# Kernel optimization log

Measured on AMD Instinct MI355X. Metric: run time of the kernel, lower is better.

Reference implementation:

```python
import jax, jax.numpy as jnp
import numpy as np

N_NODES = 100000
N_EDGES = 1600000
N_GRAPHS = 64
IN_DIM = 128
HIDDEN = 64
OUT_DIM = 6


def gcn_conv(x, W, b, src, dst, n_nodes):
    """PyG GCNConv: D^{-1/2} (A + I) D^{-1/2} X W + b (self-loops added)."""
    xw = x @ W  # [N, H]
    # degree including self-loop (computed over destination nodes)
    deg = jax.ops.segment_sum(jnp.ones((src.shape[0],), xw.dtype), dst,
                              num_segments=n_nodes) + 1.0
    dinv = jax.lax.rsqrt(deg)  # deg >= 1, always safe
    # per-edge normalized messages, scatter-add into destinations
    coef = (dinv[src] * dinv[dst])[:, None]  # [E, 1]
    agg = jax.ops.segment_sum(xw[src] * coef, dst, num_segments=n_nodes)
    # self-loop contribution: dinv[i]^2 * xw[i]
    agg = agg + xw * (dinv * dinv)[:, None]
    return agg + b


def setup_inputs() -> dict:
    key = jax.random.key(0)
    ks = jax.random.split(key, 9)
    x = jax.random.normal(ks[0], (N_NODES, IN_DIM), dtype=jnp.float32)
    edge_index = jax.random.randint(ks[1], (2, N_EDGES), 0, N_NODES, dtype=jnp.int64)
    batch = jnp.sort(jax.random.randint(ks[2], (N_NODES,), 0, N_GRAPHS, dtype=jnp.int64))
    # Glorot-ish params
    W1 = jax.random.normal(ks[3], (IN_DIM, HIDDEN), dtype=jnp.float32) / np.sqrt(IN_DIM)
    b1 = jnp.zeros((HIDDEN,), jnp.float32)
    W2 = jax.random.normal(ks[4], (HIDDEN, HIDDEN), dtype=jnp.float32) / np.sqrt(HIDDEN)
    b2 = jnp.zeros((HIDDEN,), jnp.float32)
    Wl = jax.random.normal(ks[5], (HIDDEN, OUT_DIM), dtype=jnp.float32) / np.sqrt(HIDDEN)
    bl = jnp.zeros((OUT_DIM,), jnp.float32)
    return {"x": x, "edge_index": edge_index, "batch": batch,
            "W1": W1, "b1": b1, "W2": W2, "b2": b2, "Wl": Wl, "bl": bl}


def reference(x, edge_index, batch, W1, b1, W2, b2, Wl, bl):
    src, dst = edge_index[0], edge_index[1]
    h = jax.nn.relu(gcn_conv(x, W1, b1, src, dst, N_NODES))
    # dropout is identity in eval mode
    h = gcn_conv(h, W2, b2, src, dst, N_NODES)
    # global mean pool over graph ids
    sums = jax.ops.segment_sum(h, batch, num_segments=N_GRAPHS)  # [G, H]
    cnts = jax.ops.segment_sum(jnp.ones((h.shape[0],), h.dtype), batch,
                               num_segments=N_GRAPHS)
    pooled = sums / jnp.maximum(cnts, 1.0)[:, None]
    return pooled @ Wl + bl  # [G, OUT_DIM]
```

## Files before the change

### kernel.cpp

```cpp
#include <hip/hip_runtime.h>

#define NCOL 64
#define BSH 8
#define NBMAX 512
#define EPB 2048
#define P2CAP 6144


__device__ __forceinline__ unsigned int bf16pair(float a, float b) {
  unsigned int ua = __float_as_uint(a), ub = __float_as_uint(b);
  ua = (ua + 0x7FFFu + ((ua >> 16) & 1u)) >> 16;
  ub = (ub + 0x7FFFu + ((ub >> 16) & 1u)) >> 16;
  return (ub << 16) | ua;
}
__device__ __forceinline__ float bf_lo(unsigned int v) { return __uint_as_float(v << 16); }
__device__ __forceinline__ float bf_hi(unsigned int v) { return __uint_as_float(v & 0xFFFF0000u); }


__global__ __launch_bounds__(256) void bin_p1(const int* __restrict__ src,
                                              const int* __restrict__ dst,
                                              unsigned int* __restrict__ ent,
                                              int* __restrict__ blockOff,
                                              int ne, int nb) {
  __shared__ int hist[NBMAX];
  __shared__ int base[NBMAX];
  __shared__ int part[256];
  __shared__ unsigned int stage[EPB];
  int tid = threadIdx.x;
  int e0 = blockIdx.x * EPB;
  int cnt = min(EPB, ne - e0);

  for (int i = tid; i < NBMAX; i += 256) hist[i] = 0;
  __syncthreads();
  for (int i = tid; i < cnt; i += 256) {
    int d = dst[e0 + i];
    atomicAdd(&hist[d >> BSH], 1);
  }
  __syncthreads();

  int a0 = hist[2 * tid], a1 = hist[2 * tid + 1];
  int s = a0 + a1;
  part[tid] = s;
  __syncthreads();
  for (int d = 1; d < 256; d <<= 1) {
    int v = (tid >= d) ? part[tid - d] : 0;
    __syncthreads();
    part[tid] += v;
    __syncthreads();
  }
  int off = part[tid] - s;
  base[2 * tid] = off;
  base[2 * tid + 1] = off + a0;
  __syncthreads();

  for (int b = tid; b < nb; b += 256) blockOff[(size_t)blockIdx.x * nb + b] = base[b];
  for (int i = tid; i < NBMAX; i += 256) hist[i] = base[i];
  __syncthreads();

  for (int i = tid; i < cnt; i += 256) {
    int d = dst[e0 + i];
    int sv = src[e0 + i];
    unsigned int e = ((unsigned int)(d & ((1 << BSH) - 1)) << 17) | (unsigned int)sv;
    int p = atomicAdd(&hist[d >> BSH], 1);
    stage[p] = e;
  }
  __syncthreads();
  for (int i = tid; i < cnt; i += 256) ent[e0 + i] = stage[i];
}


__global__ __launch_bounds__(256) void deg_bin(const unsigned int* __restrict__ ent,
                                               const int* __restrict__ blockOff,
                                               int* __restrict__ degi,
                                               int n, int ne, int nb, int nblk) {
  __shared__ int cnt[256];
  int b = blockIdx.x;
  int tid = threadIdx.x;
  cnt[tid] = 0;
  __syncthreads();
  for (int blk = tid; blk < nblk; blk += 256) {
    int e0 = blk * EPB;
    int bcnt = min(EPB, ne - e0);
    int st = blockOff[(size_t)blk * nb + b];
    int en = (b + 1 < nb) ? blockOff[(size_t)blk * nb + b + 1] : bcnt;
    for (int i = st; i < en; ++i) {
      unsigned int e = ent[e0 + i];
      atomicAdd(&cnt[e >> 17], 1);
    }
  }
  __syncthreads();
  int node = (b << BSH) + tid;
  if (node < n) degi[node] = cnt[tid];
}

__global__ void dinv_kernel(const int* __restrict__ degi, float* __restrict__ dinv, int n) {
  int i = blockIdx.x * blockDim.x + threadIdx.x;
  if (i < n) dinv[i] = rsqrtf((float)degi[i] + 1.0f);
}


__global__ void bounds_kernel(const int* __restrict__ batch, int* __restrict__ startg,
                              int* __restrict__ endg, int n) {
  int i = blockIdx.x * blockDim.x + threadIdx.x;
  if (i >= n) return;
  int b = batch[i];
  if (i == 0) {
    startg[b] = 0;
  } else {
    int bp = batch[i - 1];
    if (b != bp) { startg[b] = i; endg[bp] = i; }
  }
  if (i == n - 1) endg[b] = n;
}


#define SCAN_C 8

__global__ void scan_part(const int* __restrict__ degi, int* __restrict__ tsum,
                          int n, int nthreads) {
  int t = blockIdx.x * blockDim.x + threadIdx.x;
  if (t >= nthreads) return;
  int lo = t * SCAN_C, hi = min(lo + SCAN_C, n);
  int s = 0;
  for (int i = lo; i < hi; ++i) s += degi[i];
  tsum[t] = s;
}

__global__ void scan_mid(int* __restrict__ tsum, int* __restrict__ toff, int nthreads) {
  __shared__ int part[1024];
  int t = threadIdx.x;
  int chunk = (nthreads + 1023) >> 10;
  int lo = t * chunk, hi = min(lo + chunk, nthreads);
  int s = 0;
  for (int i = lo; i < hi; ++i) s += tsum[i];
  part[t] = s;
  __syncthreads();
  for (int d = 1; d < 1024; d <<= 1) {
    int v = (t >= d) ? part[t - d] : 0;
    __syncthreads();
    part[t] += v;
    __syncthreads();
  }
  int off = part[t] - s;
  for (int i = lo; i < hi; ++i) { toff[i] = off; off += tsum[i]; }
}

__global__ void scan_fill(const int* __restrict__ degi, const int* __restrict__ toff,
                          int* __restrict__ rowptr, int n, int nthreads) {
  int t = blockIdx.x * blockDim.x + threadIdx.x;
  if (t >= nthreads) return;
  int lo = t * SCAN_C, hi = min(lo + SCAN_C, n);
  int off = toff[t];
  for (int i = lo; i < hi; ++i) {
    rowptr[i] = off;
    off += degi[i];
  }
  if (hi == n) rowptr[n] = off;
}


__global__ __launch_bounds__(256) void bin_p2(const unsigned int* __restrict__ ent,
                                              const int* __restrict__ blockOff,
                                              const int* __restrict__ rowptr,
                                              int* __restrict__ csr_src,
                                              int n, int ne, int nb, int nblk) {
  __shared__ int cur[256];
  __shared__ int outS[P2CAP];
  int b = blockIdx.x;
  int tid = threadIdx.x;
  int node0 = b << BSH;
  int node1 = min(node0 + 256, n);
  int bucketBase = rowptr[node0];
  int bucketCnt = rowptr[node1] - bucketBase;
  int node = node0 + tid;
  cur[tid] = (node < node1) ? (rowptr[node] - bucketBase) : 0;
  __syncthreads();
  for (int blk = tid; blk < nblk; blk += 256) {
    int e0 = blk * EPB;
    int bcnt = min(EPB, ne - e0);
    int st = blockOff[(size_t)blk * nb + b];
    int en = (b + 1 < nb) ? blockOff[(size_t)blk * nb + b + 1] : bcnt;
    for (int i = st; i < en; ++i) {
      unsigned int e = ent[e0 + i];
      int dL = e >> 17;
      int sv = (int)(e & 0x1FFFFu);
      int p = atomicAdd(&cur[dL], 1);
      if (p < P2CAP) outS[p] = sv;
      else csr_src[bucketBase + p] = sv;
    }
  }
  __syncthreads();
  int lim = min(bucketCnt, P2CAP);
  for (int i = tid; i < lim; i += 256) csr_src[bucketBase + i] = outS[i];
}


template<int K>
__global__ __launch_bounds__(256, 8) void gemm_tiled(
    const float* __restrict__ X, const float* __restrict__ W,
    const float* __restrict__ dinv, unsigned int* __restrict__ Ybf, int n) {
  __shared__ float XS[64][65];
  int tid = threadIdx.x;
  int rows0 = blockIdx.x * 64;
  int lane = tid & 63;
  int cgrp = __builtin_amdgcn_readfirstlane(tid >> 6);
  int gr = rows0 + lane;

  float acc[16];
#pragma unroll
  for (int c = 0; c < 16; ++c) acc[c] = 0.f;

  for (int ks = 0; ks < K; ks += 64) {
    if (ks) __syncthreads();
    int r0 = tid >> 4;
    int c4 = (tid & 15) * 4;
#pragma unroll
    for (int it = 0; it < 4; ++it) {
      int r = r0 + it * 16;
      int gr2 = min(rows0 + r, n - 1);
      float4 v = *reinterpret_cast<const float4*>(X + (size_t)gr2 * K + ks + c4);
      XS[r][c4 + 0] = v.x; XS[r][c4 + 1] = v.y;
      XS[r][c4 + 2] = v.z; XS[r][c4 + 3] = v.w;
    }
    __syncthreads();

    const float* wbase = W + (size_t)ks * NCOL + cgrp * 16;
#pragma unroll 4
    for (int k = 0; k < 64; ++k) {
      float xk = XS[lane][k];
      const float* wr = wbase + (size_t)k * NCOL;
#pragma unroll
      for (int c = 0; c < 16; c += 4) {
        float4 wv = *reinterpret_cast<const float4*>(wr + c);
        acc[c + 0] = fmaf(xk, wv.x, acc[c + 0]);
        acc[c + 1] = fmaf(xk, wv.y, acc[c + 1]);
        acc[c + 2] = fmaf(xk, wv.z, acc[c + 2]);
        acc[c + 3] = fmaf(xk, wv.w, acc[c + 3]);
      }
    }
  }

  if (gr < n) {
    float d = dinv[gr];
    unsigned int* yr = Ybf + (size_t)gr * (NCOL / 2) + cgrp * 8;
    uint4 o0, o1;
    o0.x = bf16pair(acc[0] * d,  acc[1] * d);
    o0.y = bf16pair(acc[2] * d,  acc[3] * d);
    o0.z = bf16pair(acc[4] * d,  acc[5] * d);
    o0.w = bf16pair(acc[6] * d,  acc[7] * d);
    o1.x = bf16pair(acc[8] * d,  acc[9] * d);
    o1.y = bf16pair(acc[10] * d, acc[11] * d);
    o1.z = bf16pair(acc[12] * d, acc[13] * d);
    o1.w = bf16pair(acc[14] * d, acc[15] * d);
    *reinterpret_cast<uint4*>(yr) = o0;
    *reinterpret_cast<uint4*>(yr + 4) = o1;
  }
}


template<bool RELU>
__global__ __launch_bounds__(256) void aggregate(
    const int* __restrict__ rowptr, const int* __restrict__ csr_src,
    const uint4* __restrict__ Ybf4, const float* __restrict__ dinv,
    const float* __restrict__ bias, float* __restrict__ H, int n) {
  int nd = (blockIdx.x * blockDim.x + threadIdx.x) >> 3;
  if (nd >= n) return;
  int l = threadIdx.x & 7;
  int lo = rowptr[nd], hi = rowptr[nd + 1];

  uint4 vs = Ybf4[(size_t)nd * 8 + l];
  float a0 = bf_lo(vs.x), a1 = bf_hi(vs.x);
  float a2 = bf_lo(vs.y), a3 = bf_hi(vs.y);
  float a4 = bf_lo(vs.z), a5 = bf_hi(vs.z);
  float a6 = bf_lo(vs.w), a7 = bf_hi(vs.w);

  int p = lo;
  for (; p + 1 < hi; p += 2) {
    int s0 = csr_src[p];
    int s1 = csr_src[p + 1];
    uint4 v0 = Ybf4[(size_t)s0 * 8 + l];
    uint4 v1 = Ybf4[(size_t)s1 * 8 + l];
    a0 += bf_lo(v0.x); a1 += bf_hi(v0.x);
    a2 += bf_lo(v0.y); a3 += bf_hi(v0.y);
    a4 += bf_lo(v0.z); a5 += bf_hi(v0.z);
    a6 += bf_lo(v0.w); a7 += bf_hi(v0.w);
    a0 += bf_lo(v1.x); a1 += bf_hi(v1.x);
    a2 += bf_lo(v1.y); a3 += bf_hi(v1.y);
    a4 += bf_lo(v1.z); a5 += bf_hi(v1.z);
    a6 += bf_lo(v1.w); a7 += bf_hi(v1.w);
  }
  if (p < hi) {
    int s = csr_src[p];
    uint4 v = Ybf4[(size_t)s * 8 + l];
    a0 += bf_lo(v.x); a1 += bf_hi(v.x);
    a2 += bf_lo(v.y); a3 += bf_hi(v.y);
    a4 += bf_lo(v.z); a5 += bf_hi(v.z);
    a6 += bf_lo(v.w); a7 += bf_hi(v.w);
  }

  float d = dinv[nd];
  float4 b0 = *reinterpret_cast<const float4*>(bias + l * 8);
  float4 b1 = *reinterpret_cast<const float4*>(bias + l * 8 + 4);
  float4 o0, o1;
  o0.x = fmaf(d, a0, b0.x); o0.y = fmaf(d, a1, b0.y);
  o0.z = fmaf(d, a2, b0.z); o0.w = fmaf(d, a3, b0.w);
  o1.x = fmaf(d, a4, b1.x); o1.y = fmaf(d, a5, b1.y);
  o1.z = fmaf(d, a6, b1.z); o1.w = fmaf(d, a7, b1.w);
  if (RELU) {
    o0.x = fmaxf(o0.x, 0.f); o0.y = fmaxf(o0.y, 0.f);
    o0.z = fmaxf(o0.z, 0.f); o0.w = fmaxf(o0.w, 0.f);
    o1.x = fmaxf(o1.x, 0.f); o1.y = fmaxf(o1.y, 0.f);
    o1.z = fmaxf(o1.z, 0.f); o1.w = fmaxf(o1.w, 0.f);
  }
  float* hr = H + (size_t)nd * NCOL + l * 8;
  *reinterpret_cast<float4*>(hr) = o0;
  *reinterpret_cast<float4*>(hr + 4) = o1;
}


#define NPG 64

__global__ void pool_kernel(const float* __restrict__ H, const int* __restrict__ batch,
                            float* __restrict__ pool, int n) {
  int gid = (blockIdx.x * blockDim.x + threadIdx.x) >> 6;
  int c = threadIdx.x & 63;
  int n0 = gid * NPG;
  if (n0 >= n) return;
  int n1 = min(n0 + NPG, n);
  float acc = 0.f;
  int curg = batch[n0];
  for (int nd = n0; nd < n1; ++nd) {
    int g = batch[nd];
    if (g != curg) {
      atomicAdd(&pool[(size_t)curg * NCOL + c], acc);
      acc = 0.f;
      curg = g;
    }
    acc += H[(size_t)nd * NCOL + c];
  }
  atomicAdd(&pool[(size_t)curg * NCOL + c], acc);
}


__global__ void final_kernel(const float* __restrict__ pool, const int* __restrict__ startg,
                             const int* __restrict__ endg, const float* __restrict__ Wl,
                             const float* __restrict__ bl, float* __restrict__ out, int ng) {
  int t = threadIdx.x;
  if (t >= ng * 6) return;
  int g = t / 6, o = t % 6;
  float cntf = (float)(endg[g] - startg[g]);
  float inv = 1.0f / fmaxf(cntf, 1.0f);
  float s = 0.f;
#pragma unroll
  for (int c = 0; c < NCOL; ++c) s += pool[(size_t)g * NCOL + c] * Wl[c * 6 + o];
  out[t] = fmaf(s, inv, bl[o]);
}


extern "C" void kernel_launch(void* const* d_in, const int* in_sizes, int n_in,
                              void* d_out, int out_size, void* d_ws, size_t ws_size,
                              hipStream_t stream) {
  const float* x    = (const float*)d_in[0];
  const int*   ei   = (const int*)d_in[1];
  const int*   batch= (const int*)d_in[2];
  const float* W1   = (const float*)d_in[3];
  const float* b1   = (const float*)d_in[4];
  const float* W2   = (const float*)d_in[5];
  const float* b2   = (const float*)d_in[6];
  const float* Wl   = (const float*)d_in[7];
  const float* bl   = (const float*)d_in[8];
  float* out = (float*)d_out;

  int n  = in_sizes[0] / 128;
  int ne = in_sizes[1] / 2;
  int ng = out_size / 6;
  const int* srcI = ei;
  const int* dstI = ei + ne;

  int nb   = (n + 255) >> BSH;
  int nblk = (ne + EPB - 1) / EPB;

  char* w = (char*)d_ws;
  size_t o = 0;
  auto take = [&](size_t bytes) -> char* {
    char* p = w + o;
    o = (o + bytes + 255) & ~(size_t)255;
    return p;
  };
  float*        dinv    = (float*)take((size_t)n * 4);
  int*          degi    = (int*)  take((size_t)n * 4);
  int*          rowptr  = (int*)  take((size_t)(n + 1) * 4);
  int*          csr_src = (int*)  take((size_t)ne * 4);
  unsigned int* ent     = (unsigned int*)take((size_t)ne * 4);
  int*          blockOff= (int*)  take((size_t)nblk * nb * 4);
  unsigned int* Ybf     = (unsigned int*)take((size_t)n * (NCOL / 2) * 4);
  float*        H       = (float*)take((size_t)n * NCOL * 4);
  float*        pool    = (float*)take(4096 * 4);
  int*          startg  = (int*)  take(64 * 4);
  int*          endg    = (int*)  take(64 * 4);
  int*          tsum    = (int*)  take(16384 * 4);
  int*          toff    = (int*)  take(16384 * 4);

  hipMemsetAsync(pool, 0, 4096 * 4, stream);
  hipMemsetAsync(startg, 0, 64 * 4, stream);
  hipMemsetAsync(endg, 0, 64 * 4, stream);

  int nb256 = (n + 255) / 256;
  int nthreads = (n + SCAN_C - 1) / SCAN_C;
  int nbScan = (nthreads + 255) / 256;

  bin_p1<<<nblk, 256, 0, stream>>>(srcI, dstI, ent, blockOff, ne, nb);
  deg_bin<<<nb, 256, 0, stream>>>(ent, blockOff, degi, n, ne, nb, nblk);
  bounds_kernel<<<nb256, 256, 0, stream>>>(batch, startg, endg, n);
  dinv_kernel<<<nb256, 256, 0, stream>>>(degi, dinv, n);
  scan_part<<<nbScan, 256, 0, stream>>>(degi, tsum, n, nthreads);
  scan_mid<<<1, 1024, 0, stream>>>(tsum, toff, nthreads);
  scan_fill<<<nbScan, 256, 0, stream>>>(degi, toff, rowptr, n, nthreads);
  bin_p2<<<nb, 256, 0, stream>>>(ent, blockOff, rowptr, csr_src, n, ne, nb, nblk);

  int nbAgg = (n * 8 + 255) / 256;
  int nbGemm = (n + 63) / 64;

  gemm_tiled<128><<<nbGemm, 256, 0, stream>>>(x, W1, dinv, Ybf, n);
  aggregate<true><<<nbAgg, 256, 0, stream>>>(rowptr, csr_src, (const uint4*)Ybf, dinv, b1, H, n);

  gemm_tiled<64><<<nbGemm, 256, 0, stream>>>(H, W2, dinv, Ybf, n);
  aggregate<false><<<nbAgg, 256, 0, stream>>>(rowptr, csr_src, (const uint4*)Ybf, dinv, b2, H, n);

  int ngroups = (n + NPG - 1) / NPG;
  int pblocks = (ngroups * 64 + 255) / 256;
  pool_kernel<<<pblocks, 256, 0, stream>>>(H, batch, pool, n);
  final_kernel<<<1, 384, 0, stream>>>(pool, startg, endg, Wl, bl, out, ng);
}
```

Before: 237.0 us.

## Stage weights in LDS with 4x4 register tiles in GEMM; unroll gather by four

The GEMM now loads each 64-row slice of W into shared memory alongside the X tile. Each thread computes a 4x4 output micro-tile from LDS, where before every thread read W directly from global memory for 16 columns of one row. Separately, the aggregate loop now issues four neighbour gathers per iteration instead of two, to keep more memory loads in flight. The price is more LDS per block, a lower occupancy hint (launch_bounds 8 to 4), higher register pressure, and narrower 8-byte output stores.

```diff
diff --git a/kernel.cpp b/kernel.cpp
--- a/kernel.cpp
+++ b/kernel.cpp
@@ -196,24 +196,27 @@
 
 
 template<int K>
-__global__ __launch_bounds__(256, 8) void gemm_tiled(
+__global__ __launch_bounds__(256, 4) void gemm_tiled(
     const float* __restrict__ X, const float* __restrict__ W,
     const float* __restrict__ dinv, unsigned int* __restrict__ Ybf, int n) {
   __shared__ float XS[64][65];
+  __shared__ float WS[64][68];
   int tid = threadIdx.x;
   int rows0 = blockIdx.x * 64;
-  int lane = tid & 63;
-  int cgrp = __builtin_amdgcn_readfirstlane(tid >> 6);
-  int gr = rows0 + lane;
-
-  float acc[16];
+  int tr = tid & 15;
+  int tc = tid >> 4;
+
+  float acc[4][4];
 #pragma unroll
-  for (int c = 0; c < 16; ++c) acc[c] = 0.f;
+  for (int i = 0; i < 4; ++i)
+#pragma unroll
+    for (int j = 0; j < 4; ++j) acc[i][j] = 0.f;
+
+  int r0 = tid >> 4;
+  int c4 = (tid & 15) * 4;
 
   for (int ks = 0; ks < K; ks += 64) {
     if (ks) __syncthreads();
-    int r0 = tid >> 4;
-    int c4 = (tid & 15) * 4;
 #pragma unroll
     for (int it = 0; it < 4; ++it) {
       int r = r0 + it * 16;
@@ -221,39 +224,49 @@
       float4 v = *reinterpret_cast<const float4*>(X + (size_t)gr2 * K + ks + c4);
       XS[r][c4 + 0] = v.x; XS[r][c4 + 1] = v.y;
       XS[r][c4 + 2] = v.z; XS[r][c4 + 3] = v.w;
+      float4 wv = *reinterpret_cast<const float4*>(W + (size_t)(ks + r) * NCOL + c4);
+      WS[r][c4 + 0] = wv.x; WS[r][c4 + 1] = wv.y;
+      WS[r][c4 + 2] = wv.z; WS[r][c4 + 3] = wv.w;
     }
     __syncthreads();
 
-    const float* wbase = W + (size_t)ks * NCOL + cgrp * 16;
 #pragma unroll 4
-    for (int k = 0; k < 64; ++k) {
-      float xk = XS[lane][k];
-      const float* wr = wbase + (size_t)k * NCOL;
+    for (int k = 0; k < 64; k += 2) {
+      float a0 = XS[4 * tr + 0][k], a1 = XS[4 * tr + 1][k];
+      float a2 = XS[4 * tr + 2][k], a3 = XS[4 * tr + 3][k];
+      float b0 = XS[4 * tr + 0][k + 1], b1 = XS[4 * tr + 1][k + 1];
+      float b2 = XS[4 * tr + 2][k + 1], b3 = XS[4 * tr + 3][k + 1];
+      float4 w0 = *reinterpret_cast<const float4*>(&WS[k][4 * tc]);
+      float4 w1 = *reinterpret_cast<const float4*>(&WS[k + 1][4 * tc]);
+      acc[0][0] = fmaf(a0, w0.x, acc[0][0]); acc[0][1] = fmaf(a0, w0.y, acc[0][1]);
+      acc[0][2] = fmaf(a0, w0.z, acc[0][2]); acc[0][3] = fmaf(a0, w0.w, acc[0][3]);
+      acc[1][0] = fmaf(a1, w0.x, acc[1][0]); acc[1][1] = fmaf(a1, w0.y, acc[1][1]);
+      acc[1][2] = fmaf(a1, w0.z, acc[1][2]); acc[1][3] = fmaf(a1, w0.w, acc[1][3]);
+      acc[2][0] = fmaf(a2, w0.x, acc[2][0]); acc[2][1] = fmaf(a2, w0.y, acc[2][1]);
+      acc[2][2] = fmaf(a2, w0.z, acc[2][2]); acc[2][3] = fmaf(a2, w0.w, acc[2][3]);
+      acc[3][0] = fmaf(a3, w0.x, acc[3][0]); acc[3][1] = fmaf(a3, w0.y, acc[3][1]);
+      acc[3][2] = fmaf(a3, w0.z, acc[3][2]); acc[3][3] = fmaf(a3, w0.w, acc[3][3]);
+      acc[0][0] = fmaf(b0, w1.x, acc[0][0]); acc[0][1] = fmaf(b0, w1.y, acc[0][1]);
+      acc[0][2] = fmaf(b0, w1.z, acc[0][2]); acc[0][3] = fmaf(b0, w1.w, acc[0][3]);
+      acc[1][0] = fmaf(b1, w1.x, acc[1][0]); acc[1][1] = fmaf(b1, w1.y, acc[1][1]);
+      acc[1][2] = fmaf(b1, w1.z, acc[1][2]); acc[1][3] = fmaf(b1, w1.w, acc[1][3]);
+      acc[2][0] = fmaf(b2, w1.x, acc[2][0]); acc[2][1] = fmaf(b2, w1.y, acc[2][1]);
+      acc[2][2] = fmaf(b2, w1.z, acc[2][2]); acc[2][3] = fmaf(b2, w1.w, acc[2][3]);
+      acc[3][0] = fmaf(b3, w1.x, acc[3][0]); acc[3][1] = fmaf(b3, w1.y, acc[3][1]);
+      acc[3][2] = fmaf(b3, w1.z, acc[3][2]); acc[3][3] = fmaf(b3, w1.w, acc[3][3]);
+    }
+  }
+
 #pragma unroll
-      for (int c = 0; c < 16; c += 4) {
-        float4 wv = *reinterpret_cast<const float4*>(wr + c);
-        acc[c + 0] = fmaf(xk, wv.x, acc[c + 0]);
-        acc[c + 1] = fmaf(xk, wv.y, acc[c + 1]);
-        acc[c + 2] = fmaf(xk, wv.z, acc[c + 2]);
-        acc[c + 3] = fmaf(xk, wv.w, acc[c + 3]);
-      }
-    }
-  }
-
-  if (gr < n) {
-    float d = dinv[gr];
-    unsigned int* yr = Ybf + (size_t)gr * (NCOL / 2) + cgrp * 8;
-    uint4 o0, o1;
-    o0.x = bf16pair(acc[0] * d,  acc[1] * d);
-    o0.y = bf16pair(acc[2] * d,  acc[3] * d);
-    o0.z = bf16pair(acc[4] * d,  acc[5] * d);
-    o0.w = bf16pair(acc[6] * d,  acc[7] * d);
-    o1.x = bf16pair(acc[8] * d,  acc[9] * d);
-    o1.y = bf16pair(acc[10] * d, acc[11] * d);
-    o1.z = bf16pair(acc[12] * d, acc[13] * d);
-    o1.w = bf16pair(acc[14] * d, acc[15] * d);
-    *reinterpret_cast<uint4*>(yr) = o0;
-    *reinterpret_cast<uint4*>(yr + 4) = o1;
+  for (int i = 0; i < 4; ++i) {
+    int gr = rows0 + 4 * tr + i;
+    if (gr < n) {
+      float d = dinv[gr];
+      uint2 o;
+      o.x = bf16pair(acc[i][0] * d, acc[i][1] * d);
+      o.y = bf16pair(acc[i][2] * d, acc[i][3] * d);
+      *reinterpret_cast<uint2*>(Ybf + (size_t)gr * (NCOL / 2) + 2 * tc) = o;
+    }
   }
 }
 
@@ -275,11 +288,15 @@
   float a6 = bf_lo(vs.w), a7 = bf_hi(vs.w);
 
   int p = lo;
-  for (; p + 1 < hi; p += 2) {
+  for (; p + 3 < hi; p += 4) {
     int s0 = csr_src[p];
     int s1 = csr_src[p + 1];
+    int s2 = csr_src[p + 2];
+    int s3 = csr_src[p + 3];
     uint4 v0 = Ybf4[(size_t)s0 * 8 + l];
     uint4 v1 = Ybf4[(size_t)s1 * 8 + l];
+    uint4 v2 = Ybf4[(size_t)s2 * 8 + l];
+    uint4 v3 = Ybf4[(size_t)s3 * 8 + l];
     a0 += bf_lo(v0.x); a1 += bf_hi(v0.x);
     a2 += bf_lo(v0.y); a3 += bf_hi(v0.y);
     a4 += bf_lo(v0.z); a5 += bf_hi(v0.z);
@@ -288,8 +305,16 @@
     a2 += bf_lo(v1.y); a3 += bf_hi(v1.y);
     a4 += bf_lo(v1.z); a5 += bf_hi(v1.z);
     a6 += bf_lo(v1.w); a7 += bf_hi(v1.w);
-  }
-  if (p < hi) {
+    a0 += bf_lo(v2.x); a1 += bf_hi(v2.x);
+    a2 += bf_lo(v2.y); a3 += bf_hi(v2.y);
+    a4 += bf_lo(v2.z); a5 += bf_hi(v2.z);
+    a6 += bf_lo(v2.w); a7 += bf_hi(v2.w);
+    a0 += bf_lo(v3.x); a1 += bf_hi(v3.x);
+    a2 += bf_lo(v3.y); a3 += bf_hi(v3.y);
+    a4 += bf_lo(v3.z); a5 += bf_hi(v3.z);
+    a6 += bf_lo(v3.w); a7 += bf_hi(v3.w);
+  }
+  for (; p < hi; ++p) {
     int s = csr_src[p];
     uint4 v = Ybf4[(size_t)s * 8 + l];
     a0 += bf_lo(v.x); a1 += bf_hi(v.x);
```

Measured after the change: 240.5 us. Within noise of the previous version (+1.5%).
